# Performance work log

Hardware: AMD Instinct MI355X
Metric: run time of the kernel (lower is better)

The kernel has to match this reference:

```python
import jax, jax.numpy as jnp
import numpy as np

B, T, D, H = 4, 2048, 512, 8
DH = D // H


def setup_inputs() -> dict:
    key = jax.random.key(0)
    ks = jax.random.split(key, 13)
    s = 1.0 / np.sqrt(D)
    inp = {
        "q": jax.random.normal(ks[0], (B, T, D), jnp.float32),
        "k": jax.random.normal(ks[1], (B, T, D), jnp.float32),
        "v": jax.random.normal(ks[2], (B, T, D), jnp.float32),
        # key padding mask, broadcastable to [B, H, T_q, T_k]; mostly True
        "padding_mask": jax.random.uniform(ks[3], (B, 1, 1, T)) > 0.1,
        "W_q": jax.random.normal(ks[4], (D, D), jnp.float32) * s,
        "b_q": jnp.zeros((D,), jnp.float32),
        "W_k": jax.random.normal(ks[5], (D, D), jnp.float32) * s,
        "b_k": jnp.zeros((D,), jnp.float32),
        "W_v": jax.random.normal(ks[6], (D, D), jnp.float32) * s,
        "b_v": jnp.zeros((D,), jnp.float32),
        "W_o": jax.random.normal(ks[7], (D, D), jnp.float32) * s,
        "b_o": jnp.zeros((D,), jnp.float32),
    }
    return inp


def reference(q, k, v, padding_mask, W_q, b_q, W_k, b_k, W_v, b_v, W_o, b_o):
    # Linear projections, then split heads: [B, T, D] -> [B, H, T, DH]
    def heads(x, W, b):
        y = x @ W + b
        return y.reshape(x.shape[0], x.shape[1], H, DH).transpose(0, 2, 1, 3)

    Q = heads(q, W_q, b_q)
    K = heads(k, W_k, b_k)
    V = heads(v, W_v, b_v)

    scores = jnp.einsum("bhqd,bhkd->bhqk", Q, K) / jnp.sqrt(jnp.float32(DH))
    scores = jnp.where(padding_mask, scores, -jnp.inf)
    weights = jax.nn.softmax(scores, axis=-1)
    weights = jnp.nan_to_num(weights, nan=0.0)  # all-masked rows -> 0
    x = jnp.einsum("bhqk,bhkd->bhqd", weights, V)
    x = x.transpose(0, 2, 1, 3).reshape(q.shape[0], q.shape[1], D)
    return x @ W_o + b_o
```

## Files before the change

### kernel.cpp

```cpp
#include <hip/hip_runtime.h>
#include <hip/hip_bf16.h>
#include <math.h>


#define TB 2048
#define DD 512
#define NH 8
#define DH 64

typedef short bf16x8 __attribute__((ext_vector_type(8)));
typedef float f32x4 __attribute__((ext_vector_type(4)));

static __device__ __forceinline__ ushort f2bf(float x) {
  __hip_bfloat16 h = __float2bfloat16(x);
  return *reinterpret_cast<ushort*>(&h);
}
static __device__ __forceinline__ float bf2f(ushort u) {
  unsigned int v = ((unsigned int)u) << 16;
  return __uint_as_float(v);
}
static __device__ __forceinline__ float fast_exp2(float x) {
  return __builtin_amdgcn_exp2f(x);
}
static __device__ __forceinline__ unsigned pack2(float x, float y) {
  return __builtin_amdgcn_perm(__float_as_uint(y) + 0x8000u,
                               __float_as_uint(x) + 0x8000u, 0x07060302u);
}
static __device__ __forceinline__ bf16x8 cvt8(float4 lo, float4 hi) {
  union { unsigned u[4]; bf16x8 v; } r;
  r.u[0] = pack2(lo.x, lo.y);
  r.u[1] = pack2(lo.z, lo.w);
  r.u[2] = pack2(hi.x, hi.y);
  r.u[3] = pack2(hi.z, hi.w);
  return r.v;
}

__global__ void mask_detect_kernel(const unsigned char* __restrict__ m,
                                   int* __restrict__ mode) {
  __shared__ int c1, c2;
  if (threadIdx.x == 0) { c1 = 0; c2 = 0; }
  __syncthreads();
  int l1 = 0, l2 = 0;
  for (int i = threadIdx.x; i < 8192; i += blockDim.x) {
    int ph = i & 3;
    unsigned char v = m[i];
    if (ph == 1 && v) l1++;
    if (ph == 2 && v) l2++;
  }
  if (l1) atomicAdd(&c1, l1);
  if (l2) atomicAdd(&c2, l2);
  __syncthreads();
  if (threadIdx.x == 0) *mode = (c1 > 0) ? 0 : ((c2 > 0) ? 1 : 2);
}

__global__ void mask_build_kernel(const void* __restrict__ m,
                                  const int* __restrict__ mode,
                                  float* __restrict__ out) {
  int i = blockIdx.x * blockDim.x + threadIdx.x;
  int md = *mode;
  int v;
  if (md == 0)      v = ((const unsigned char*)m)[i] != 0;
  else if (md == 1) v = ((const float*)m)[i] != 0.0f;
  else              v = ((const int*)m)[i] != 0;
  out[i] = v ? 0.0f : -INFINITY;
}

__global__ __launch_bounds__(256) void wtrans3_kernel(
    const float* __restrict__ Wq, const float* __restrict__ Wk,
    const float* __restrict__ Wv, ushort* __restrict__ Wall) {
  __shared__ ushort t[64][68];
  const float* W = (blockIdx.z == 0) ? Wq : (blockIdx.z == 1) ? Wk : Wv;
  ushort* Wt = Wall + (size_t)blockIdx.z * (512 * 512);
  const int bn = blockIdx.x << 6, bk = blockIdx.y << 6;
  const int tx = threadIdx.x & 15, ty = threadIdx.x >> 4;
#pragma unroll
  for (int rr = 0; rr < 64; rr += 16) {
    float4 v = *(const float4*)&W[(size_t)(bk + rr + ty) * DD + bn + (tx << 2)];
    t[(tx << 2) + 0][rr + ty] = f2bf(v.x);
    t[(tx << 2) + 1][rr + ty] = f2bf(v.y);
    t[(tx << 2) + 2][rr + ty] = f2bf(v.z);
    t[(tx << 2) + 3][rr + ty] = f2bf(v.w);
  }
  __syncthreads();
#pragma unroll
  for (int rr = 0; rr < 64; rr += 16) {
    ushort4 o;
    o.x = t[rr + ty][(tx << 2) + 0];
    o.y = t[rr + ty][(tx << 2) + 1];
    o.z = t[rr + ty][(tx << 2) + 2];
    o.w = t[rr + ty][(tx << 2) + 3];
    *(ushort4*)&Wt[(size_t)(bn + rr + ty) * DD + bk + (tx << 2)] = o;
  }
}

__global__ __launch_bounds__(256) void wtrans_split_kernel(
    const float* __restrict__ W, ushort* __restrict__ Wt) {
  __shared__ ushort thi[64][68];
  __shared__ ushort tlo[64][68];
  const int bn = blockIdx.x << 6, bk = blockIdx.y << 6;
  const int tx = threadIdx.x & 15, ty = threadIdx.x >> 4;
#pragma unroll
  for (int rr = 0; rr < 64; rr += 16) {
    float4 v = *(const float4*)&W[(size_t)(bk + rr + ty) * DD + bn + (tx << 2)];
    float vv[4] = {v.x, v.y, v.z, v.w};
#pragma unroll
    for (int c = 0; c < 4; ++c) {
      ushort hi = f2bf(vv[c]);
      ushort lo = f2bf(vv[c] - bf2f(hi));
      thi[(tx << 2) + c][rr + ty] = hi;
      tlo[(tx << 2) + c][rr + ty] = lo;
    }
  }
  __syncthreads();
#pragma unroll
  for (int rr = 0; rr < 64; rr += 16) {
    ushort4 h4, l4;
    h4.x = thi[rr + ty][(tx << 2) + 0];
    h4.y = thi[rr + ty][(tx << 2) + 1];
    h4.z = thi[rr + ty][(tx << 2) + 2];
    h4.w = thi[rr + ty][(tx << 2) + 3];
    l4.x = tlo[rr + ty][(tx << 2) + 0];
    l4.y = tlo[rr + ty][(tx << 2) + 1];
    l4.z = tlo[rr + ty][(tx << 2) + 2];
    l4.w = tlo[rr + ty][(tx << 2) + 3];
    size_t rowb = (size_t)(bn + rr + ty) * 1536;
    *(ushort4*)&Wt[rowb + bk + (tx << 2)] = h4;
    *(ushort4*)&Wt[rowb + 512 + bk + (tx << 2)] = h4;
    *(ushort4*)&Wt[rowb + 1024 + bk + (tx << 2)] = l4;
  }
}

__global__ __launch_bounds__(256) void projqkv_kernel(
    const float* __restrict__ Qx, const float* __restrict__ Kx,
    const float* __restrict__ Vx, const ushort* __restrict__ Wall,
    const float* __restrict__ bq, const float* __restrict__ bk,
    const float* __restrict__ bv, ushort* __restrict__ Yall, float qscale) {
  __shared__ __align__(16) ushort As[2][128][32];
  __shared__ __align__(16) ushort Bs[2][128][32];

  const int tid = threadIdx.x;
  const int w = tid >> 6, lane = tid & 63;
  const int llo = lane & 15, lhi = lane >> 4;
  const int wm = w >> 1, wn = w & 1;

  const int bid = blockIdx.x;
  const int x = bid & 7, rest = bid >> 3;
  const int ni = rest & 3;
  const int gg = (rest >> 2) * 8 + x;
  const int sec = gg >> 6;
  const int mt = gg & 63;
  const int m0 = mt << 7;
  const int n0s = ni << 7;

  const float* A = (sec == 0) ? Qx : (sec == 1) ? Kx : Vx;
  const float* bias = (sec == 0) ? bq : (sec == 1) ? bk : bv;
  const float scale = (sec == 0) ? qscale : 1.0f;
  const ushort* Wt = Wall + (size_t)(sec * 512 + n0s) * DD;

  const int srow = tid >> 1, scol = (tid & 1) << 4;
  const float* Ag = A + (size_t)(m0 + srow) * DD + scol;
  const ushort* Bg = Wt + (size_t)srow * DD + scol;

  f32x4 acc[4][4];
#pragma unroll
  for (int mi = 0; mi < 4; ++mi)
#pragma unroll
    for (int nj = 0; nj < 4; ++nj) acc[mi][nj] = (f32x4){0.f, 0.f, 0.f, 0.f};

  {
    float4 f0 = *(const float4*)(Ag + 0);
    float4 f1 = *(const float4*)(Ag + 4);
    float4 f2 = *(const float4*)(Ag + 8);
    float4 f3 = *(const float4*)(Ag + 12);
    bf16x8 w0 = *(const bf16x8*)(Bg + 0);
    bf16x8 w1 = *(const bf16x8*)(Bg + 8);
    *(bf16x8*)&As[0][srow][scol] = cvt8(f0, f1);
    *(bf16x8*)&As[0][srow][scol + 8] = cvt8(f2, f3);
    *(bf16x8*)&Bs[0][srow][scol] = w0;
    *(bf16x8*)&Bs[0][srow][scol + 8] = w1;
  }
  __syncthreads();

  int cur = 0;
  for (int t = 0; t < 16; ++t) {
    float4 f0, f1, f2, f3;
    bf16x8 w0, w1;
    if (t < 15) {
      const float* ag = Ag + (t + 1) * 32;
      const ushort* bg = Bg + (t + 1) * 32;
      f0 = *(const float4*)(ag + 0);
      f1 = *(const float4*)(ag + 4);
      f2 = *(const float4*)(ag + 8);
      f3 = *(const float4*)(ag + 12);
      w0 = *(const bf16x8*)(bg + 0);
      w1 = *(const bf16x8*)(bg + 8);
    }
    bf16x8 af[4], bfr[4];
#pragma unroll
    for (int mi = 0; mi < 4; ++mi)
      af[mi] = *(const bf16x8*)&As[cur][wm * 64 + mi * 16 + llo][lhi * 8];
#pragma unroll
    for (int nj = 0; nj < 4; ++nj)
      bfr[nj] = *(const bf16x8*)&Bs[cur][wn * 64 + nj * 16 + llo][lhi * 8];
    __builtin_amdgcn_s_setprio(1);
#pragma unroll
    for (int mi = 0; mi < 4; ++mi)
#pragma unroll
      for (int nj = 0; nj < 4; ++nj)
        acc[mi][nj] = __builtin_amdgcn_mfma_f32_16x16x32_bf16(
            af[mi], bfr[nj], acc[mi][nj], 0, 0, 0);
    __builtin_amdgcn_s_setprio(0);
    if (t < 15) {
      *(bf16x8*)&As[cur ^ 1][srow][scol] = cvt8(f0, f1);
      *(bf16x8*)&As[cur ^ 1][srow][scol + 8] = cvt8(f2, f3);
      *(bf16x8*)&Bs[cur ^ 1][srow][scol] = w0;
      *(bf16x8*)&Bs[cur ^ 1][srow][scol + 8] = w1;
    }
    __syncthreads();
    cur ^= 1;
  }

  float bb[4];
#pragma unroll
  for (int nj = 0; nj < 4; ++nj)
    bb[nj] = bias[n0s + wn * 64 + nj * 16 + llo];

  ushort* Yq = Yall;
  ushort* Yk = Yall + ((size_t)4 << 20);
  ushort* Yv = Yall + ((size_t)8 << 20);
#pragma unroll
  for (int mi = 0; mi < 4; ++mi)
#pragma unroll
    for (int nj = 0; nj < 4; ++nj) {
      int colS = n0s + wn * 64 + nj * 16 + llo;
      int h = colS >> 6, dh = colS & (DH - 1);
#pragma unroll
      for (int r = 0; r < 4; ++r) {
        int row = m0 + wm * 64 + mi * 16 + lhi * 4 + r;
        int bidx = row >> 11, t = row & (TB - 1);
        int bh = bidx * NH + h;
        ushort u = f2bf((acc[mi][nj][r] + bb[nj]) * scale);
        if (sec == 0) {
          Yq[((size_t)(bh * 128 + (t >> 4)) * 2 + (dh >> 5)) * 512 +
             ((((dh >> 3) & 3) << 4) + (t & 15)) * 8 + (dh & 7)] = u;
        } else if (sec == 1) {
          Yk[((size_t)(bh * 32 + (t >> 6)) << 12) +
             (((dh >> 5) << 2) + ((t >> 4) & 3)) * 512 +
             ((((dh >> 3) & 3) << 4) + (t & 15)) * 8 + (dh & 7)] = u;
        } else {
          Yv[((size_t)(bh * 32 + (t >> 6)) << 12) +
             ((((t >> 5) & 1) << 2) + (dh >> 4)) * 512 +
             ((((t >> 3) & 3) << 4) + (dh & 15)) * 8 + (t & 7)] = u;
        }
      }
    }
}

__global__ __launch_bounds__(256) void projo_kernel(
    const ushort* __restrict__ A, const ushort* __restrict__ Wt,
    const float* __restrict__ bias, float* __restrict__ Y) {
  __shared__ __align__(16) ushort As[2][128][32];
  __shared__ __align__(16) ushort Bs[2][64][32];

  const int tid = threadIdx.x;
  const int w = tid >> 6, lane = tid & 63;
  const int llo = lane & 15, lhi = lane >> 4;
  const int wm = w >> 1, wn = w & 1;

  const int bid = blockIdx.x;
  const int x = bid & 7, rest = bid >> 3;
  const int ni = rest & 7;
  const int mt = (rest >> 3) * 8 + x;
  const int m0 = mt << 7;
  const int n0 = ni << 6;
  const int K = 1536;

  const int arow = tid >> 1, acol = (tid & 1) << 4;
  const int brow = tid >> 2, bcol = (tid & 3) << 3;
  const ushort* Ag = A + (size_t)(m0 + arow) * K + acol;
  const ushort* Bg = Wt + (size_t)(n0 + brow) * K + bcol;

  f32x4 acc[4][2];
#pragma unroll
  for (int mi = 0; mi < 4; ++mi)
#pragma unroll
    for (int nj = 0; nj < 2; ++nj) acc[mi][nj] = (f32x4){0.f, 0.f, 0.f, 0.f};

  {
    bf16x8 a0 = *(const bf16x8*)(Ag + 0);
    bf16x8 a1 = *(const bf16x8*)(Ag + 8);
    bf16x8 b0 = *(const bf16x8*)(Bg + 0);
    *(bf16x8*)&As[0][arow][acol] = a0;
    *(bf16x8*)&As[0][arow][acol + 8] = a1;
    *(bf16x8*)&Bs[0][brow][bcol] = b0;
  }
  __syncthreads();

  int cur = 0;
#pragma unroll 2
  for (int t = 0; t < 48; ++t) {
    bf16x8 a0, a1, b0;
    if (t < 47) {
      const ushort* ag = Ag + (t + 1) * 32;
      const ushort* bg = Bg + (t + 1) * 32;
      a0 = *(const bf16x8*)(ag + 0);
      a1 = *(const bf16x8*)(ag + 8);
      b0 = *(const bf16x8*)(bg + 0);
    }
    bf16x8 af[4], bfr[2];
#pragma unroll
    for (int mi = 0; mi < 4; ++mi)
      af[mi] = *(const bf16x8*)&As[cur][wm * 64 + mi * 16 + llo][lhi * 8];
#pragma unroll
    for (int nj = 0; nj < 2; ++nj)
      bfr[nj] = *(const bf16x8*)&Bs[cur][wn * 32 + nj * 16 + llo][lhi * 8];
    __builtin_amdgcn_s_setprio(1);
#pragma unroll
    for (int mi = 0; mi < 4; ++mi)
#pragma unroll
      for (int nj = 0; nj < 2; ++nj)
        acc[mi][nj] = __builtin_amdgcn_mfma_f32_16x16x32_bf16(
            af[mi], bfr[nj], acc[mi][nj], 0, 0, 0);
    __builtin_amdgcn_s_setprio(0);
    if (t < 47) {
      *(bf16x8*)&As[cur ^ 1][arow][acol] = a0;
      *(bf16x8*)&As[cur ^ 1][arow][acol + 8] = a1;
      *(bf16x8*)&Bs[cur ^ 1][brow][bcol] = b0;
    }
    __syncthreads();
    cur ^= 1;
  }

  float bb[2];
#pragma unroll
  for (int nj = 0; nj < 2; ++nj)
    bb[nj] = bias[n0 + wn * 32 + nj * 16 + llo];
#pragma unroll
  for (int mi = 0; mi < 4; ++mi)
#pragma unroll
    for (int nj = 0; nj < 2; ++nj) {
      int col = n0 + wn * 32 + nj * 16 + llo;
#pragma unroll
      for (int r = 0; r < 4; ++r) {
        int row = m0 + wm * 64 + mi * 16 + lhi * 4 + r;
        Y[(size_t)row * DD + col] = acc[mi][nj][r] + bb[nj];
      }
    }
}

__global__ __launch_bounds__(256) void attn_mfma_kernel(
    const ushort* __restrict__ Qf,
    const ushort* __restrict__ Kf,
    const ushort* __restrict__ Vf,
    const float* __restrict__ mbias,
    ushort* __restrict__ Ap) {
  __shared__ __align__(16) ushort Plds[4][16][72];

  const int tid = threadIdx.x;
  const int w = tid >> 6, lane = tid & 63;
  const int lhi = lane >> 4, llo = lane & 15;
  const int lane8 = lane * 8;

  const int bid = blockIdx.x;
  const int j = bid >> 3;
  const int bh = (bid & 7) + ((j >> 5) << 3);
  const int qt = j & 31;
  const int b = bh >> 3, h = bh & 7;
  const int q0 = qt << 6;

  const float* mb = mbias + b * TB;
  ushort* pl = &Plds[w][0][0];

  const ushort* Qb = Qf + ((size_t)((bh << 7) + (q0 >> 4) + w) * 2) * 512 + lane8;
  bf16x8 qa0 = *(const bf16x8*)Qb;
  bf16x8 qa1 = *(const bf16x8*)(Qb + 512);

  const size_t bhK = (size_t)bh << 5;
  f32x4 oacc[4];
#pragma unroll
  for (int nt = 0; nt < 4; ++nt) oacc[nt] = (f32x4){0.f, 0.f, 0.f, 0.f};
  float m = -INFINITY, l = 0.f;

  bf16x8 kf[8];
  {
    const ushort* Kt0 = Kf + (bhK << 12) + lane8;
#pragma unroll
    for (int i = 0; i < 8; ++i) kf[i] = *(const bf16x8*)(Kt0 + i * 512);
  }

  for (int kt64 = 0; kt64 < 32; ++kt64) {
    const ushort* Vt = Vf + ((bhK + kt64) << 12) + lane8;
    bf16x8 vf[8];
#pragma unroll
    for (int i = 0; i < 8; ++i) vf[i] = *(const bf16x8*)(Vt + i * 512);
    float4 mb4[4];
#pragma unroll
    for (int nt = 0; nt < 4; ++nt)
      mb4[nt] = *(const float4*)&mb[kt64 * 64 + nt * 16 + lhi * 4];

    f32x4 s[4];
    __builtin_amdgcn_s_setprio(1);
#pragma unroll
    for (int nt = 0; nt < 4; ++nt) {
      s[nt] = (f32x4){0.f, 0.f, 0.f, 0.f};
      s[nt] = __builtin_amdgcn_mfma_f32_16x16x32_bf16(kf[nt], qa0, s[nt], 0, 0, 0);
      s[nt] = __builtin_amdgcn_mfma_f32_16x16x32_bf16(kf[4 + nt], qa1, s[nt], 0, 0, 0);
    }
    __builtin_amdgcn_s_setprio(0);

    {
      const ushort* Ktn = Kf + ((bhK + ((kt64 + 1) & 31)) << 12) + lane8;
#pragma unroll
      for (int i = 0; i < 8; ++i) kf[i] = *(const bf16x8*)(Ktn + i * 512);
    }

#pragma unroll
    for (int nt = 0; nt < 4; ++nt) {
      s[nt][0] += mb4[nt].x;
      s[nt][1] += mb4[nt].y;
      s[nt][2] += mb4[nt].z;
      s[nt][3] += mb4[nt].w;
    }

    float mx[4];
#pragma unroll
    for (int nt = 0; nt < 4; ++nt)
      mx[nt] = fmaxf(fmaxf(s[nt][0], s[nt][1]), fmaxf(s[nt][2], s[nt][3]));
    float lmax = fmaxf(fmaxf(mx[0], mx[1]), fmaxf(mx[2], mx[3]));

    if (__any(lmax > m + 8.f)) {
      float rmax = fmaxf(lmax, __shfl_xor(lmax, 16));
      rmax = fmaxf(rmax, __shfl_xor(rmax, 32));
      float newm = fmaxf(m, rmax);
      float alpha = (newm == -INFINITY) ? 0.f : fast_exp2(m - newm);
      float al[4];
#pragma unroll
      for (int r = 0; r < 4; ++r) al[r] = __shfl(alpha, lhi * 4 + r);
#pragma unroll
      for (int nt = 0; nt < 4; ++nt) {
        oacc[nt][0] *= al[0];
        oacc[nt][1] *= al[1];
        oacc[nt][2] *= al[2];
        oacc[nt][3] *= al[3];
      }
      l *= alpha;
      m = newm;
    }

#pragma unroll
    for (int nt = 0; nt < 4; ++nt)
#pragma unroll
      for (int r = 0; r < 4; ++r) s[nt][r] = fast_exp2(s[nt][r] - m);
    if (__any(m == -INFINITY)) {
      if (m == -INFINITY) {
#pragma unroll
        for (int nt = 0; nt < 4; ++nt) s[nt] = (f32x4){0.f, 0.f, 0.f, 0.f};
      }
    }
    float sm[4];
#pragma unroll
    for (int nt = 0; nt < 4; ++nt)
      sm[nt] = (s[nt][0] + s[nt][1]) + (s[nt][2] + s[nt][3]);
    l += (sm[0] + sm[1]) + (sm[2] + sm[3]);

#pragma unroll
    for (int nt = 0; nt < 4; ++nt) {
      unsigned int lo = pack2(s[nt][0], s[nt][1]);
      unsigned int hi = pack2(s[nt][2], s[nt][3]);
      *(uint2*)&pl[llo * 72 + nt * 16 + lhi * 4] = make_uint2(lo, hi);
    }

    __builtin_amdgcn_s_setprio(1);
#pragma unroll
    for (int kc = 0; kc < 2; ++kc) {
      bf16x8 pa = *(const bf16x8*)&pl[llo * 72 + kc * 32 + lhi * 8];
#pragma unroll
      for (int nt = 0; nt < 4; ++nt)
        oacc[nt] = __builtin_amdgcn_mfma_f32_16x16x32_bf16(pa, vf[kc * 4 + nt], oacc[nt], 0, 0, 0);
    }
    __builtin_amdgcn_s_setprio(0);
  }

  l += __shfl_xor(l, 16);
  l += __shfl_xor(l, 32);
  float linv = (l > 0.f) ? 1.f / l : 0.f;
  float il[4];
#pragma unroll
  for (int r = 0; r < 4; ++r) il[r] = __shfl(linv, lhi * 4 + r);
  const int t0 = q0 + w * 16 + lhi * 4;
#pragma unroll
  for (int r = 0; r < 4; ++r) {
    size_t rowb = (size_t)(b * TB + t0 + r) * 1536;
#pragma unroll
    for (int nt = 0; nt < 4; ++nt) {
      float o = oacc[nt][r] * il[r];
      ushort hi = f2bf(o);
      ushort lo = f2bf(o - bf2f(hi));
      int c = h * DH + nt * 16 + llo;
      Ap[rowb + c] = hi;
      Ap[rowb + 512 + c] = lo;
      Ap[rowb + 1024 + c] = hi;
    }
  }
}

extern "C" void kernel_launch(void* const* d_in, const int* in_sizes, int n_in,
                              void* d_out, int out_size, void* d_ws,
                              size_t ws_size, hipStream_t stream) {
  (void)in_sizes; (void)n_in; (void)out_size; (void)ws_size;
  const float* q = (const float*)d_in[0];
  const float* k = (const float*)d_in[1];
  const float* v = (const float*)d_in[2];
  const void* pm = d_in[3];
  const float* Wq = (const float*)d_in[4];
  const float* bq = (const float*)d_in[5];
  const float* Wk = (const float*)d_in[6];
  const float* bk = (const float*)d_in[7];
  const float* Wv = (const float*)d_in[8];
  const float* bv = (const float*)d_in[9];
  const float* Wo = (const float*)d_in[10];
  const float* bo = (const float*)d_in[11];

  char* ws = (char*)d_ws;
  const size_t MB = (size_t)1 << 20;
  ushort* Ap = (ushort*)(ws);
  ushort* Wall = (ushort*)(ws + 24 * MB);
  ushort* Wot = (ushort*)(ws + 26 * MB);
  ushort* Qh = (ushort*)(ws + 32 * MB);
  float* mbias = (float*)(ws + 56 * MB);
  int* mode = (int*)(ws + 56 * MB + 40960);

  mask_detect_kernel<<<1, 256, 0, stream>>>((const unsigned char*)pm, mode);
  mask_build_kernel<<<32, 256, 0, stream>>>(pm, mode, mbias);

  wtrans3_kernel<<<dim3(8, 8, 3), 256, 0, stream>>>(Wq, Wk, Wv, Wall);
  wtrans_split_kernel<<<dim3(8, 8), 256, 0, stream>>>(Wo, Wot);

  const float qscale = 0.125f * 1.4426950408889634f;
  projqkv_kernel<<<768, 256, 0, stream>>>(q, k, v, Wall,
                                          bq, bk, bv, Qh, qscale);

  attn_mfma_kernel<<<1024, 256, 0, stream>>>(
      Qh, Qh + ((size_t)4 << 20), Qh + ((size_t)8 << 20), mbias, Ap);

  projo_kernel<<<512, 256, 0, stream>>>(Ap, Wot, bo, (float*)d_out);
}
```

Before: 159.8 us.

## Split attention KV range across two waves per query tile and merge in LDS

Each block now runs 8 waves instead of 4. Each pair of waves shares a 16-row query tile, and each wave in the pair processes half of the 32 key/value chunks (split-K flash attention). The partial outputs and the per-row max and sum values are written to shared memory, then combined with rescaling before the normalized result is stored to global memory as vectorized ushort4 writes. This doubles the wave-level parallelism and halves the serial loop length per wave. The cost is a larger LDS footprint, a block-wide barrier and an extra combine pass.

```diff
diff --git a/kernel.cpp b/kernel.cpp
--- a/kernel.cpp
+++ b/kernel.cpp
@@ -348,18 +348,21 @@
     }
 }
 
-__global__ __launch_bounds__(256) void attn_mfma_kernel(
+__global__ __launch_bounds__(512) void attn_mfma_kernel(
     const ushort* __restrict__ Qf,
     const ushort* __restrict__ Kf,
     const ushort* __restrict__ Vf,
     const float* __restrict__ mbias,
     ushort* __restrict__ Ap) {
-  __shared__ __align__(16) ushort Plds[4][16][72];
+  __shared__ __align__(16) ushort Plds[8][16][72];
+  __shared__ __align__(16) float Ow[8][16][64];
+  __shared__ float Ml[8][2][16];
 
   const int tid = threadIdx.x;
   const int w = tid >> 6, lane = tid & 63;
   const int lhi = lane >> 4, llo = lane & 15;
   const int lane8 = lane * 8;
+  const int qg = w >> 1, half = w & 1;
 
   const int bid = blockIdx.x;
   const int j = bid >> 3;
@@ -371,7 +374,8 @@
   const float* mb = mbias + b * TB;
   ushort* pl = &Plds[w][0][0];
 
-  const ushort* Qb = Qf + ((size_t)((bh << 7) + (q0 >> 4) + w) * 2) * 512 + lane8;
+  const ushort* Qb =
+      Qf + ((size_t)((bh << 7) + (q0 >> 4) + qg) * 2) * 512 + lane8;
   bf16x8 qa0 = *(const bf16x8*)Qb;
   bf16x8 qa1 = *(const bf16x8*)(Qb + 512);
 
@@ -381,14 +385,17 @@
   for (int nt = 0; nt < 4; ++nt) oacc[nt] = (f32x4){0.f, 0.f, 0.f, 0.f};
   float m = -INFINITY, l = 0.f;
 
+  const int base = half << 4;
+
   bf16x8 kf[8];
   {
-    const ushort* Kt0 = Kf + (bhK << 12) + lane8;
+    const ushort* Kt0 = Kf + ((bhK + base) << 12) + lane8;
 #pragma unroll
     for (int i = 0; i < 8; ++i) kf[i] = *(const bf16x8*)(Kt0 + i * 512);
   }
 
-  for (int kt64 = 0; kt64 < 32; ++kt64) {
+  for (int rel = 0; rel < 16; ++rel) {
+    const int kt64 = base + rel;
     const ushort* Vt = Vf + ((bhK + kt64) << 12) + lane8;
     bf16x8 vf[8];
 #pragma unroll
@@ -409,7 +416,8 @@
     __builtin_amdgcn_s_setprio(0);
 
     {
-      const ushort* Ktn = Kf + ((bhK + ((kt64 + 1) & 31)) << 12) + lane8;
+      const int ktn = base + ((rel + 1) & 15);
+      const ushort* Ktn = Kf + ((bhK + ktn) << 12) + lane8;
 #pragma unroll
       for (int i = 0; i < 8; ++i) kf[i] = *(const bf16x8*)(Ktn + i * 512);
     }
@@ -483,24 +491,47 @@
 
   l += __shfl_xor(l, 16);
   l += __shfl_xor(l, 32);
-  float linv = (l > 0.f) ? 1.f / l : 0.f;
-  float il[4];
-#pragma unroll
-  for (int r = 0; r < 4; ++r) il[r] = __shfl(linv, lhi * 4 + r);
-  const int t0 = q0 + w * 16 + lhi * 4;
-#pragma unroll
-  for (int r = 0; r < 4; ++r) {
-    size_t rowb = (size_t)(b * TB + t0 + r) * 1536;
-#pragma unroll
-    for (int nt = 0; nt < 4; ++nt) {
-      float o = oacc[nt][r] * il[r];
-      ushort hi = f2bf(o);
-      ushort lo = f2bf(o - bf2f(hi));
-      int c = h * DH + nt * 16 + llo;
-      Ap[rowb + c] = hi;
-      Ap[rowb + 512 + c] = lo;
-      Ap[rowb + 1024 + c] = hi;
-    }
+#pragma unroll
+  for (int nt = 0; nt < 4; ++nt)
+#pragma unroll
+    for (int r = 0; r < 4; ++r)
+      Ow[w][lhi * 4 + r][nt * 16 + llo] = oacc[nt][r];
+  if (lane < 16) {
+    Ml[w][0][llo] = m;
+    Ml[w][1][llo] = l;
+  }
+  __syncthreads();
+
+#pragma unroll
+  for (int rep = 0; rep < 2; ++rep) {
+    int item = tid + rep * 512;
+    int row = item >> 4;
+    int d4 = (item & 15) << 2;
+    int g = row >> 4, qr = row & 15;
+    int w0 = g * 2, w1 = g * 2 + 1;
+    float m0 = Ml[w0][0][qr], m1 = Ml[w1][0][qr];
+    float M = fmaxf(m0, m1);
+    ushort4 h4 = {0, 0, 0, 0}, l4 = {0, 0, 0, 0};
+    if (M != -INFINITY) {
+      float e0 = fast_exp2(m0 - M), e1 = fast_exp2(m1 - M);
+      float den = Ml[w0][1][qr] * e0 + Ml[w1][1][qr] * e1;
+      float4 o0 = *(const float4*)&Ow[w0][qr][d4];
+      float4 o1 = *(const float4*)&Ow[w1][qr][d4];
+      float inv = (den > 0.f) ? 1.f / den : 0.f;
+      float ox = (o0.x * e0 + o1.x * e1) * inv;
+      float oy = (o0.y * e0 + o1.y * e1) * inv;
+      float oz = (o0.z * e0 + o1.z * e1) * inv;
+      float ow = (o0.w * e0 + o1.w * e1) * inv;
+      h4.x = f2bf(ox); l4.x = f2bf(ox - bf2f(h4.x));
+      h4.y = f2bf(oy); l4.y = f2bf(oy - bf2f(h4.y));
+      h4.z = f2bf(oz); l4.z = f2bf(oz - bf2f(h4.z));
+      h4.w = f2bf(ow); l4.w = f2bf(ow - bf2f(h4.w));
+    }
+    size_t rowb = (size_t)(b * TB + q0 + row) * 1536;
+    int c = h * DH + d4;
+    *(ushort4*)&Ap[rowb + c] = h4;
+    *(ushort4*)&Ap[rowb + 512 + c] = l4;
+    *(ushort4*)&Ap[rowb + 1024 + c] = h4;
   }
 }
 
@@ -540,7 +571,7 @@
   projqkv_kernel<<<768, 256, 0, stream>>>(q, k, v, Wall,
                                           bq, bk, bv, Qh, qscale);
 
-  attn_mfma_kernel<<<1024, 256, 0, stream>>>(
+  attn_mfma_kernel<<<1024, 512, 0, stream>>>(
       Qh, Qh + ((size_t)4 << 20), Qh + ((size_t)8 << 20), mbias, Ap);
 
   projo_kernel<<<512, 256, 0, stream>>>(Ap, Wot, bo, (float*)d_out);
```

Measured after the change: 172.7 us. 1.08x slower.

## Process two 16-row query tiles per wave to reuse K/V fragments

Applied to the files above, without the earlier changes.

Each wave now handles 32 query rows as two independent online-softmax streams (A and B) that share the same K and V register fragments loaded per 64-key tile. The block covers 128 queries and the grid is halved, cutting K/V global loads per query in half. The K prefetch across iterations is dropped in favour of in-loop loads. This raises register pressure and reduces the number of blocks, which may hurt occupancy and latency hiding.

```diff
diff --git a/kernel.cpp b/kernel.cpp
--- a/kernel.cpp
+++ b/kernel.cpp
@@ -354,7 +354,7 @@
     const ushort* __restrict__ Vf,
     const float* __restrict__ mbias,
     ushort* __restrict__ Ap) {
-  __shared__ __align__(16) ushort Plds[4][16][72];
+  __shared__ __align__(16) ushort Plds[4][2][16][72];
 
   const int tid = threadIdx.x;
   const int w = tid >> 6, lane = tid & 63;
@@ -363,143 +363,211 @@
 
   const int bid = blockIdx.x;
   const int j = bid >> 3;
-  const int bh = (bid & 7) + ((j >> 5) << 3);
-  const int qt = j & 31;
+  const int bh = (bid & 7) + ((j >> 4) << 3);
+  const int qt = j & 15;
   const int b = bh >> 3, h = bh & 7;
-  const int q0 = qt << 6;
+  const int q0 = qt << 7;
 
   const float* mb = mbias + b * TB;
-  ushort* pl = &Plds[w][0][0];
-
-  const ushort* Qb = Qf + ((size_t)((bh << 7) + (q0 >> 4) + w) * 2) * 512 + lane8;
+  ushort* plA = &Plds[w][0][0][0];
+  ushort* plB = &Plds[w][1][0][0];
+
+  const ushort* Qb =
+      Qf + ((size_t)((bh << 7) + (q0 >> 4) + w * 2) * 2) * 512 + lane8;
   bf16x8 qa0 = *(const bf16x8*)Qb;
   bf16x8 qa1 = *(const bf16x8*)(Qb + 512);
+  bf16x8 qa2 = *(const bf16x8*)(Qb + 1024);
+  bf16x8 qa3 = *(const bf16x8*)(Qb + 1536);
 
   const size_t bhK = (size_t)bh << 5;
-  f32x4 oacc[4];
-#pragma unroll
-  for (int nt = 0; nt < 4; ++nt) oacc[nt] = (f32x4){0.f, 0.f, 0.f, 0.f};
-  float m = -INFINITY, l = 0.f;
-
-  bf16x8 kf[8];
-  {
-    const ushort* Kt0 = Kf + (bhK << 12) + lane8;
-#pragma unroll
-    for (int i = 0; i < 8; ++i) kf[i] = *(const bf16x8*)(Kt0 + i * 512);
-  }
+  f32x4 oaccA[4], oaccB[4];
+#pragma unroll
+  for (int nt = 0; nt < 4; ++nt) {
+    oaccA[nt] = (f32x4){0.f, 0.f, 0.f, 0.f};
+    oaccB[nt] = (f32x4){0.f, 0.f, 0.f, 0.f};
+  }
+  float mA = -INFINITY, lA = 0.f;
+  float mB = -INFINITY, lB = 0.f;
 
   for (int kt64 = 0; kt64 < 32; ++kt64) {
+    const ushort* Kt = Kf + ((bhK + kt64) << 12) + lane8;
+    bf16x8 kf[8];
+#pragma unroll
+    for (int i = 0; i < 8; ++i) kf[i] = *(const bf16x8*)(Kt + i * 512);
+    float4 mb4[4];
+#pragma unroll
+    for (int nt = 0; nt < 4; ++nt)
+      mb4[nt] = *(const float4*)&mb[kt64 * 64 + nt * 16 + lhi * 4];
+
+    f32x4 sA[4], sB[4];
+    __builtin_amdgcn_s_setprio(1);
+#pragma unroll
+    for (int nt = 0; nt < 4; ++nt) {
+      sA[nt] = (f32x4){0.f, 0.f, 0.f, 0.f};
+      sA[nt] = __builtin_amdgcn_mfma_f32_16x16x32_bf16(kf[nt], qa0, sA[nt], 0, 0, 0);
+      sA[nt] = __builtin_amdgcn_mfma_f32_16x16x32_bf16(kf[4 + nt], qa1, sA[nt], 0, 0, 0);
+    }
+#pragma unroll
+    for (int nt = 0; nt < 4; ++nt) {
+      sB[nt] = (f32x4){0.f, 0.f, 0.f, 0.f};
+      sB[nt] = __builtin_amdgcn_mfma_f32_16x16x32_bf16(kf[nt], qa2, sB[nt], 0, 0, 0);
+      sB[nt] = __builtin_amdgcn_mfma_f32_16x16x32_bf16(kf[4 + nt], qa3, sB[nt], 0, 0, 0);
+    }
+    __builtin_amdgcn_s_setprio(0);
+
     const ushort* Vt = Vf + ((bhK + kt64) << 12) + lane8;
     bf16x8 vf[8];
 #pragma unroll
     for (int i = 0; i < 8; ++i) vf[i] = *(const bf16x8*)(Vt + i * 512);
-    float4 mb4[4];
-#pragma unroll
-    for (int nt = 0; nt < 4; ++nt)
-      mb4[nt] = *(const float4*)&mb[kt64 * 64 + nt * 16 + lhi * 4];
-
-    f32x4 s[4];
+
+#pragma unroll
+    for (int nt = 0; nt < 4; ++nt) {
+      sA[nt][0] += mb4[nt].x; sB[nt][0] += mb4[nt].x;
+      sA[nt][1] += mb4[nt].y; sB[nt][1] += mb4[nt].y;
+      sA[nt][2] += mb4[nt].z; sB[nt][2] += mb4[nt].z;
+      sA[nt][3] += mb4[nt].w; sB[nt][3] += mb4[nt].w;
+    }
+
+    {
+      float mx0 = fmaxf(fmaxf(sA[0][0], sA[0][1]), fmaxf(sA[0][2], sA[0][3]));
+      float mx1 = fmaxf(fmaxf(sA[1][0], sA[1][1]), fmaxf(sA[1][2], sA[1][3]));
+      float mx2 = fmaxf(fmaxf(sA[2][0], sA[2][1]), fmaxf(sA[2][2], sA[2][3]));
+      float mx3 = fmaxf(fmaxf(sA[3][0], sA[3][1]), fmaxf(sA[3][2], sA[3][3]));
+      float lmax = fmaxf(fmaxf(mx0, mx1), fmaxf(mx2, mx3));
+      if (__any(lmax > mA + 8.f)) {
+        float rmax = fmaxf(lmax, __shfl_xor(lmax, 16));
+        rmax = fmaxf(rmax, __shfl_xor(rmax, 32));
+        float newm = fmaxf(mA, rmax);
+        float alpha = (newm == -INFINITY) ? 0.f : fast_exp2(mA - newm);
+        float al[4];
+#pragma unroll
+        for (int r = 0; r < 4; ++r) al[r] = __shfl(alpha, lhi * 4 + r);
+#pragma unroll
+        for (int nt = 0; nt < 4; ++nt) {
+          oaccA[nt][0] *= al[0];
+          oaccA[nt][1] *= al[1];
+          oaccA[nt][2] *= al[2];
+          oaccA[nt][3] *= al[3];
+        }
+        lA *= alpha;
+        mA = newm;
+      }
+#pragma unroll
+      for (int nt = 0; nt < 4; ++nt)
+#pragma unroll
+        for (int r = 0; r < 4; ++r) sA[nt][r] = fast_exp2(sA[nt][r] - mA);
+      if (__any(mA == -INFINITY)) {
+        if (mA == -INFINITY) {
+#pragma unroll
+          for (int nt = 0; nt < 4; ++nt) sA[nt] = (f32x4){0.f, 0.f, 0.f, 0.f};
+        }
+      }
+      float s0 = (sA[0][0] + sA[0][1]) + (sA[0][2] + sA[0][3]);
+      float s1 = (sA[1][0] + sA[1][1]) + (sA[1][2] + sA[1][3]);
+      float s2 = (sA[2][0] + sA[2][1]) + (sA[2][2] + sA[2][3]);
+      float s3 = (sA[3][0] + sA[3][1]) + (sA[3][2] + sA[3][3]);
+      lA += (s0 + s1) + (s2 + s3);
+#pragma unroll
+      for (int nt = 0; nt < 4; ++nt) {
+        unsigned int lo = pack2(sA[nt][0], sA[nt][1]);
+        unsigned int hi = pack2(sA[nt][2], sA[nt][3]);
+        *(uint2*)&plA[llo * 72 + nt * 16 + lhi * 4] = make_uint2(lo, hi);
+      }
+    }
+
+    {
+      float mx0 = fmaxf(fmaxf(sB[0][0], sB[0][1]), fmaxf(sB[0][2], sB[0][3]));
+      float mx1 = fmaxf(fmaxf(sB[1][0], sB[1][1]), fmaxf(sB[1][2], sB[1][3]));
+      float mx2 = fmaxf(fmaxf(sB[2][0], sB[2][1]), fmaxf(sB[2][2], sB[2][3]));
+      float mx3 = fmaxf(fmaxf(sB[3][0], sB[3][1]), fmaxf(sB[3][2], sB[3][3]));
+      float lmax = fmaxf(fmaxf(mx0, mx1), fmaxf(mx2, mx3));
+      if (__any(lmax > mB + 8.f)) {
+        float rmax = fmaxf(lmax, __shfl_xor(lmax, 16));
+        rmax = fmaxf(rmax, __shfl_xor(rmax, 32));
+        float newm = fmaxf(mB, rmax);
+        float alpha = (newm == -INFINITY) ? 0.f : fast_exp2(mB - newm);
+        float al[4];
+#pragma unroll
+        for (int r = 0; r < 4; ++r) al[r] = __shfl(alpha, lhi * 4 + r);
+#pragma unroll
+        for (int nt = 0; nt < 4; ++nt) {
+          oaccB[nt][0] *= al[0];
+          oaccB[nt][1] *= al[1];
+          oaccB[nt][2] *= al[2];
+          oaccB[nt][3] *= al[3];
+        }
+        lB *= alpha;
+        mB = newm;
+      }
+#pragma unroll
+      for (int nt = 0; nt < 4; ++nt)
+#pragma unroll
+        for (int r = 0; r < 4; ++r) sB[nt][r] = fast_exp2(sB[nt][r] - mB);
+      if (__any(mB == -INFINITY)) {
+        if (mB == -INFINITY) {
+#pragma unroll
+          for (int nt = 0; nt < 4; ++nt) sB[nt] = (f32x4){0.f, 0.f, 0.f, 0.f};
+        }
+      }
+      float s0 = (sB[0][0] + sB[0][1]) + (sB[0][2] + sB[0][3]);
+      float s1 = (sB[1][0] + sB[1][1]) + (sB[1][2] + sB[1][3]);
+      float s2 = (sB[2][0] + sB[2][1]) + (sB[2][2] + sB[2][3]);
+      float s3 = (sB[3][0] + sB[3][1]) + (sB[3][2] + sB[3][3]);
+      lB += (s0 + s1) + (s2 + s3);
+#pragma unroll
+      for (int nt = 0; nt < 4; ++nt) {
+        unsigned int lo = pack2(sB[nt][0], sB[nt][1]);
+        unsigned int hi = pack2(sB[nt][2], sB[nt][3]);
+        *(uint2*)&plB[llo * 72 + nt * 16 + lhi * 4] = make_uint2(lo, hi);
+      }
+    }
+
     __builtin_amdgcn_s_setprio(1);
 #pragma unroll
+    for (int kc = 0; kc < 2; ++kc) {
+      bf16x8 paA = *(const bf16x8*)&plA[llo * 72 + kc * 32 + lhi * 8];
+      bf16x8 paB = *(const bf16x8*)&plB[llo * 72 + kc * 32 + lhi * 8];
+#pragma unroll
+      for (int nt = 0; nt < 4; ++nt) {
+        oaccA[nt] = __builtin_amdgcn_mfma_f32_16x16x32_bf16(paA, vf[kc * 4 + nt], oaccA[nt], 0, 0, 0);
+        oaccB[nt] = __builtin_amdgcn_mfma_f32_16x16x32_bf16(paB, vf[kc * 4 + nt], oaccB[nt], 0, 0, 0);
+      }
+    }
+    __builtin_amdgcn_s_setprio(0);
+  }
+
+  lA += __shfl_xor(lA, 16);
+  lA += __shfl_xor(lA, 32);
+  lB += __shfl_xor(lB, 16);
+  lB += __shfl_xor(lB, 32);
+  float invA = (lA > 0.f) ? 1.f / lA : 0.f;
+  float invB = (lB > 0.f) ? 1.f / lB : 0.f;
+  float ilA[4], ilB[4];
+#pragma unroll
+  for (int r = 0; r < 4; ++r) {
+    ilA[r] = __shfl(invA, lhi * 4 + r);
+    ilB[r] = __shfl(invB, lhi * 4 + r);
+  }
+  const int t0 = q0 + w * 32 + lhi * 4;
+#pragma unroll
+  for (int r = 0; r < 4; ++r) {
+    size_t rowbA = (size_t)(b * TB + t0 + r) * 1536;
+    size_t rowbB = (size_t)(b * TB + t0 + 16 + r) * 1536;
+#pragma unroll
     for (int nt = 0; nt < 4; ++nt) {
-      s[nt] = (f32x4){0.f, 0.f, 0.f, 0.f};
-      s[nt] = __builtin_amdgcn_mfma_f32_16x16x32_bf16(kf[nt], qa0, s[nt], 0, 0, 0);
-      s[nt] = __builtin_amdgcn_mfma_f32_16x16x32_bf16(kf[4 + nt], qa1, s[nt], 0, 0, 0);
-    }
-    __builtin_amdgcn_s_setprio(0);
-
-    {
-      const ushort* Ktn = Kf + ((bhK + ((kt64 + 1) & 31)) << 12) + lane8;
-#pragma unroll
-      for (int i = 0; i < 8; ++i) kf[i] = *(const bf16x8*)(Ktn + i * 512);
-    }
-
-#pragma unroll
-    for (int nt = 0; nt < 4; ++nt) {
-      s[nt][0] += mb4[nt].x;
-      s[nt][1] += mb4[nt].y;
-      s[nt][2] += mb4[nt].z;
-      s[nt][3] += mb4[nt].w;
-    }
-
-    float mx[4];
-#pragma unroll
-    for (int nt = 0; nt < 4; ++nt)
-      mx[nt] = fmaxf(fmaxf(s[nt][0], s[nt][1]), fmaxf(s[nt][2], s[nt][3]));
-    float lmax = fmaxf(fmaxf(mx[0], mx[1]), fmaxf(mx[2], mx[3]));
-
-    if (__any(lmax > m + 8.f)) {
-      float rmax = fmaxf(lmax, __shfl_xor(lmax, 16));
-      rmax = fmaxf(rmax, __shfl_xor(rmax, 32));
-      float newm = fmaxf(m, rmax);
-      float alpha = (newm == -INFINITY) ? 0.f : fast_exp2(m - newm);
-      float al[4];
-#pragma unroll
-      for (int r = 0; r < 4; ++r) al[r] = __shfl(alpha, lhi * 4 + r);
-#pragma unroll
-      for (int nt = 0; nt < 4; ++nt) {
-        oacc[nt][0] *= al[0];
-        oacc[nt][1] *= al[1];
-        oacc[nt][2] *= al[2];
-        oacc[nt][3] *= al[3];
-      }
-      l *= alpha;
-      m = newm;
-    }
-
-#pragma unroll
-    for (int nt = 0; nt < 4; ++nt)
-#pragma unroll
-      for (int r = 0; r < 4; ++r) s[nt][r] = fast_exp2(s[nt][r] - m);
-    if (__any(m == -INFINITY)) {
-      if (m == -INFINITY) {
-#pragma unroll
-        for (int nt = 0; nt < 4; ++nt) s[nt] = (f32x4){0.f, 0.f, 0.f, 0.f};
-      }
-    }
-    float sm[4];
-#pragma unroll
-    for (int nt = 0; nt < 4; ++nt)
-      sm[nt] = (s[nt][0] + s[nt][1]) + (s[nt][2] + s[nt][3]);
-    l += (sm[0] + sm[1]) + (sm[2] + sm[3]);
-
-#pragma unroll
-    for (int nt = 0; nt < 4; ++nt) {
-      unsigned int lo = pack2(s[nt][0], s[nt][1]);
-      unsigned int hi = pack2(s[nt][2], s[nt][3]);
-      *(uint2*)&pl[llo * 72 + nt * 16 + lhi * 4] = make_uint2(lo, hi);
-    }
-
-    __builtin_amdgcn_s_setprio(1);
-#pragma unroll
-    for (int kc = 0; kc < 2; ++kc) {
-      bf16x8 pa = *(const bf16x8*)&pl[llo * 72 + kc * 32 + lhi * 8];
-#pragma unroll
-      for (int nt = 0; nt < 4; ++nt)
-        oacc[nt] = __builtin_amdgcn_mfma_f32_16x16x32_bf16(pa, vf[kc * 4 + nt], oacc[nt], 0, 0, 0);
-    }
-    __builtin_amdgcn_s_setprio(0);
-  }
-
-  l += __shfl_xor(l, 16);
-  l += __shfl_xor(l, 32);
-  float linv = (l > 0.f) ? 1.f / l : 0.f;
-  float il[4];
-#pragma unroll
-  for (int r = 0; r < 4; ++r) il[r] = __shfl(linv, lhi * 4 + r);
-  const int t0 = q0 + w * 16 + lhi * 4;
-#pragma unroll
-  for (int r = 0; r < 4; ++r) {
-    size_t rowb = (size_t)(b * TB + t0 + r) * 1536;
-#pragma unroll
-    for (int nt = 0; nt < 4; ++nt) {
-      float o = oacc[nt][r] * il[r];
-      ushort hi = f2bf(o);
-      ushort lo = f2bf(o - bf2f(hi));
       int c = h * DH + nt * 16 + llo;
-      Ap[rowb + c] = hi;
-      Ap[rowb + 512 + c] = lo;
-      Ap[rowb + 1024 + c] = hi;
+      float oA = oaccA[nt][r] * ilA[r];
+      ushort hiA = f2bf(oA);
+      ushort loA = f2bf(oA - bf2f(hiA));
+      Ap[rowbA + c] = hiA;
+      Ap[rowbA + 512 + c] = loA;
+      Ap[rowbA + 1024 + c] = hiA;
+      float oB = oaccB[nt][r] * ilB[r];
+      ushort hiB = f2bf(oB);
+      ushort loB = f2bf(oB - bf2f(hiB));
+      Ap[rowbB + c] = hiB;
+      Ap[rowbB + 512 + c] = loB;
+      Ap[rowbB + 1024 + c] = hiB;
     }
   }
 }
@@ -540,7 +608,7 @@
   projqkv_kernel<<<768, 256, 0, stream>>>(q, k, v, Wall,
                                           bq, bk, bv, Qh, qscale);
 
-  attn_mfma_kernel<<<1024, 256, 0, stream>>>(
+  attn_mfma_kernel<<<512, 256, 0, stream>>>(
       Qh, Qh + ((size_t)4 << 20), Qh + ((size_t)8 << 20), mbias, Ap);
 
   projo_kernel<<<512, 256, 0, stream>>>(Ap, Wot, bo, (float*)d_out);
```

New measurement: 142.1 us. 11.1% less time.
